# Performance work log

Measured on AMD Instinct MI355X. Metric: run time of the kernel, lower is better.

## Reference

```python
import jax, jax.numpy as jnp
import numpy as np

N, E, D = 50000, 800000, 128  # nodes, edges, n_feat


def setup_inputs() -> dict:
    key = jax.random.key(0)
    ks = jax.random.split(key, 12)
    scale = 1.0 / np.sqrt(D)

    def w(k):
        return jax.random.normal(k, (D, D), jnp.float32) * scale

    return {
        "h": jax.random.normal(ks[0], (N, D), jnp.float32),
        "src": jax.random.randint(ks[1], (E,), 0, N, jnp.int32),
        "dst": jax.random.randint(ks[2], (E,), 0, N, jnp.int32),
        # skip MLP: Linear -> ELU -> Linear
        "W_skip1": w(ks[3]), "b_skip1": jnp.zeros((D,), jnp.float32),
        "W_skip2": w(ks[4]), "b_skip2": jnp.zeros((D,), jnp.float32),
        # SAGEConv 1 (mean aggregator): fc_self, fc_neigh (bias-free) + shared bias
        "W_self1": w(ks[5]), "W_neigh1": w(ks[6]), "b_conv1": jnp.zeros((D,), jnp.float32),
        # self-interaction MLP
        "W_si1": w(ks[7]), "b_si1": jnp.zeros((D,), jnp.float32),
        "W_si2": w(ks[8]), "b_si2": jnp.zeros((D,), jnp.float32),
        # SAGEConv 2
        "W_self2": w(ks[9]), "W_neigh2": w(ks[10]), "b_conv2": jnp.zeros((D,), jnp.float32),
    }


def _sage_mean(h, src, dst, W_self, W_neigh, b):
    # DGL SAGEConv('mean'): fc_self(h) + fc_neigh(mean over in-neighbors of h_src) + bias
    n = h.shape[0]
    deg = jax.ops.segment_sum(jnp.ones((src.shape[0],), h.dtype), dst, num_segments=n)
    agg = jax.ops.segment_sum(h[src], dst, num_segments=n)  # [N, D] sum of neighbor feats
    agg = agg / jnp.maximum(deg, 1.0)[:, None]  # degree clamp for isolated nodes
    return h @ W_self + agg @ W_neigh + b


def reference(h, src, dst,
              W_skip1, b_skip1, W_skip2, b_skip2,
              W_self1, W_neigh1, b_conv1,
              W_si1, b_si1, W_si2, b_si2,
              W_self2, W_neigh2, b_conv2):
    elu = jax.nn.elu
    h_skip = elu(h @ W_skip1 + b_skip1) @ W_skip2 + b_skip2
    x = elu(_sage_mean(h, src, dst, W_self1, W_neigh1, b_conv1))
    x = elu(elu(x @ W_si1 + b_si1) @ W_si2 + b_si2)
    x = _sage_mean(x, src, dst, W_self2, W_neigh2, b_conv2)
    return h_skip + x
```

## Files before the change

kernel.cpp:

```cpp
#include <hip/hip_runtime.h>
#include <math.h>

#define NN 50000
#define NE 800000
#define NRT 782
#define NT  (NRT * 2)
#define NB  128
#define NPB2 391
#define EPB 2048
#define NBB 391

typedef __attribute__((ext_vector_type(8))) short short8;
typedef __attribute__((ext_vector_type(4))) float floatx4;

#define AS1 __attribute__((address_space(1)))
#define AS3 __attribute__((address_space(3)))

__device__ __forceinline__ unsigned short f2bf(float f) {
    unsigned u = __float_as_uint(f);
    unsigned r = (u + 0x7fff + ((u >> 16) & 1)) >> 16;
    return (unsigned short)r;
}
__device__ __forceinline__ float bf2f(unsigned short h) {
    return __uint_as_float(((unsigned)h) << 16);
}


__global__ __launch_bounds__(256)
void k_prep(const float* __restrict__ h, unsigned short* __restrict__ hB,
            const int* __restrict__ dst, int* __restrict__ bcnt,
            const float* w0, const float* w1, const float* w2, const float* w3,
            const float* w4, const float* w5, const float* w6, const float* w7,
            short* __restrict__ wpk) {
    int bid = blockIdx.x;
    const int t = threadIdx.x;
    if (bid < 3125) {
        int i = (bid * 256 + t) * 8;
        float4 a = *(const float4*)&h[i];
        float4 b = *(const float4*)&h[i + 4];
        short8 v;
        v[0] = (short)f2bf(a.x); v[1] = (short)f2bf(a.y);
        v[2] = (short)f2bf(a.z); v[3] = (short)f2bf(a.w);
        v[4] = (short)f2bf(b.x); v[5] = (short)f2bf(b.y);
        v[6] = (short)f2bf(b.z); v[7] = (short)f2bf(b.w);
        *(short8*)&hB[i] = v;
    } else if (bid < 3125 + NBB) {
        __shared__ int cnt[NB];
        if (t < NB) cnt[t] = 0;
        __syncthreads();
        int base = (bid - 3125) * EPB;
#pragma unroll
        for (int i = 0; i < 8; ++i) {
            int idx = base + i * 256 + t;
            if (idx < NE) atomicAdd(&cnt[dst[idx] / NPB2], 1);
        }
        __syncthreads();
        if (t < NB && cnt[t]) atomicAdd(&bcnt[t], cnt[t]);
    } else {
        int wb = bid - 3125 - NBB;
        const float* W;
        switch (wb) {
            case 0: W = w0; break; case 1: W = w1; break;
            case 2: W = w2; break; case 3: W = w3; break;
            case 4: W = w4; break; case 5: W = w5; break;
            case 6: W = w6; break; default: W = w7; break;
        }
        short* dstp = wpk + (size_t)wb * 16384;
#pragma unroll
        for (int i = 0; i < 8; ++i) {
            int q = t + i * 256;
            int cb = q >> 8, ks = (q >> 6) & 3, lane = q & 63;
            int n = lane & 15, g = lane >> 4;
            int col = cb * 16 + n, krow = ks * 32 + g * 8;
            short8 v;
#pragma unroll
            for (int j = 0; j < 8; ++j)
                v[j] = (short)f2bf(W[(krow + j) * 128 + col]);
            *(short8*)&dstp[q * 8] = v;
        }
    }
}


__global__ void k_bscan(const int* __restrict__ bcnt, int* __restrict__ gcur,
                        int* __restrict__ bstart) {
    __shared__ int s[NB];
    int t = threadIdx.x;
    int c = bcnt[t];
    s[t] = c;
    __syncthreads();
    for (int off = 1; off < NB; off <<= 1) {
        int v = (t >= off) ? s[t - off] : 0;
        __syncthreads();
        s[t] += v;
        __syncthreads();
    }
    int excl = s[t] - c;
    gcur[t] = excl;
    bstart[t] = excl;
    if (t == NB - 1) bstart[NB] = s[NB - 1];
}


__global__ __launch_bounds__(256)
void k_bucket(const int* __restrict__ src, const int* __restrict__ dst,
              int* __restrict__ gcur, int* __restrict__ bsrc, int* __restrict__ bdst) {
    __shared__ int psrc[EPB];
    __shared__ int pdst[EPB];
    __shared__ int cnt[NB];
    __shared__ int ebase[NB];
    __shared__ int gbase[NB];
    const int t = threadIdx.x;
    const int e0 = blockIdx.x * EPB;
    const int M = (e0 + EPB <= NE) ? EPB : (NE - e0);

    if (t < NB) cnt[t] = 0;
    __syncthreads();

    int es[8], ed[8], rank[8];
#pragma unroll
    for (int i = 0; i < 8; ++i) {
        int idx = i * 256 + t;
        if (idx < M) {
            es[i] = src[e0 + idx];
            ed[i] = dst[e0 + idx];
            rank[i] = atomicAdd(&cnt[ed[i] / NPB2], 1);
        }
    }
    __syncthreads();
    if (t < NB) ebase[t] = cnt[t];
    __syncthreads();
    for (int off = 1; off < NB; off <<= 1) {
        int v = 0;
        if (t < NB && t >= off) v = ebase[t - off];
        __syncthreads();
        if (t < NB) ebase[t] += v;
        __syncthreads();
    }
    if (t < NB) ebase[t] -= cnt[t];
    __syncthreads();
#pragma unroll
    for (int i = 0; i < 8; ++i) {
        int idx = i * 256 + t;
        if (idx < M) {
            int b = ed[i] / NPB2;
            int pos = ebase[b] + rank[i];
            psrc[pos] = es[i];
            pdst[pos] = ed[i];
        }
    }
    if (t < NB && cnt[t] > 0) gbase[t] = atomicAdd(&gcur[t], cnt[t]);
    __syncthreads();
#pragma unroll
    for (int i = 0; i < 8; ++i) {
        int idx = i * 256 + t;
        if (idx < M) {
            int d = pdst[idx];
            int b = d / NPB2;
            int gpos = gbase[b] + (idx - ebase[b]);
            bsrc[gpos] = psrc[idx];
            bdst[gpos] = d;
        }
    }
}


template<int DOELU, int OUTF32, int NOBIAS>
__device__ __forceinline__ void gemm_body(
        int bid, const unsigned short* __restrict__ A,
        const short* __restrict__ Wp, const float* __restrict__ bias,
        void* outv, short* sW, short* sA) {
    const int t = threadIdx.x;
    const int wv = t >> 6, lane = t & 63;
    const int rb = bid >> 1, ct = bid & 1;
    const int row0 = rb * 64, col0 = ct * 64;
    const int m = lane & 15, g = lane >> 4;

    floatx4 acc[4];
#pragma unroll
    for (int cb = 0; cb < 4; ++cb) acc[cb] = (floatx4){0.f, 0.f, 0.f, 0.f};

    const short* Wc = Wp + ct * 8192;
#pragma unroll
    for (int i = 0; i < 4; ++i) {
        int cbase = (i * 4 + wv) * 64;
        __builtin_amdgcn_global_load_lds(
            (const AS1 unsigned int*)(Wc + (size_t)(cbase + lane) * 8),
            (AS3 unsigned int*)(sW + cbase * 8), 16, 0, 0);
    }
#pragma unroll
    for (int i = 0; i < 4; ++i) {
        int cbase = (i * 4 + wv) * 64;
        int id = cbase + lane;
        int r = id >> 4, cs = id & 15;
        int rg = row0 + r; if (rg >= NN) rg = NN - 1;
        int csrc = cs ^ (r & 7);
        __builtin_amdgcn_global_load_lds(
            (const AS1 unsigned int*)(A + (size_t)rg * 128 + csrc * 8),
            (AS3 unsigned int*)(sA + cbase * 8), 16, 0, 0);
    }
    asm volatile("s_waitcnt vmcnt(0)" ::: "memory");
    __builtin_amdgcn_sched_barrier(0);
    __syncthreads();

    const int r0 = wv * 16;
#pragma unroll
    for (int ks = 0; ks < 4; ++ks) {
        int cxor = (ks * 4 + g) ^ (m & 7);
        short8 af = *(const short8*)&sA[((r0 + m) * 16 + cxor) * 8];
#pragma unroll
        for (int cb = 0; cb < 4; ++cb) {
            short8 bf = *(const short8*)&sW[((cb * 4 + ks) * 64 + lane) * 8];
            acc[cb] = __builtin_amdgcn_mfma_f32_16x16x32_bf16(af, bf, acc[cb], 0, 0, 0);
        }
    }

    const int rowbase = row0 + wv * 16 + g * 4;
#pragma unroll
    for (int cb = 0; cb < 4; ++cb) {
        int C = col0 + cb * 16 + m;
        float bb = NOBIAS ? 0.f : bias[C];
#pragma unroll
        for (int rr = 0; rr < 4; ++rr) {
            int R = rowbase + rr;
            if (R < NN) {
                size_t idx = (size_t)R * 128 + C;
                float v = acc[cb][rr] + bb;
                if (DOELU) v = (v > 0.f) ? v : expm1f(v);
                if (OUTF32) ((float*)outv)[idx] = v;
                else        ((unsigned short*)outv)[idx] = f2bf(v);
            }
        }
    }
}

template<int DOELU, int OUTF32, int NOBIAS>
__global__ __launch_bounds__(256)
void k_mm(const unsigned short* __restrict__ A, const short* __restrict__ Wp,
          const float* __restrict__ bias, void* outv) {
    __shared__ short sMem[16384];
    gemm_body<DOELU, OUTF32, NOBIAS>(blockIdx.x, A, Wp, bias, outv, sMem, sMem + 8192);
}


__device__ __forceinline__ void gemm3_body(
        int bid, const unsigned short* __restrict__ A,
        const short* __restrict__ Wn, const short* __restrict__ Ws,
        const short* __restrict__ Wk, const float* __restrict__ bsk1,
        unsigned short* __restrict__ T1, unsigned short* __restrict__ C1,
        unsigned short* __restrict__ S1, short* sW, short* sA) {
    const int t = threadIdx.x;
    const int wv = t >> 6, lane = t & 63;
    const int rb = bid >> 1, ct = bid & 1;
    const int row0 = rb * 64, col0 = ct * 64;
    const int m = lane & 15, g = lane >> 4;

#pragma unroll
    for (int i = 0; i < 4; ++i) {
        int cbase = (i * 4 + wv) * 64;
        int id = cbase + lane;
        int r = id >> 4, cs = id & 15;
        int rg = row0 + r; if (rg >= NN) rg = NN - 1;
        int csrc = cs ^ (r & 7);
        __builtin_amdgcn_global_load_lds(
            (const AS1 unsigned int*)(A + (size_t)rg * 128 + csrc * 8),
            (AS3 unsigned int*)(sA + cbase * 8), 16, 0, 0);
    }

#pragma unroll
    for (int ph = 0; ph < 3; ++ph) {
        if (ph) __syncthreads();
        const short* Wc = (ph == 0 ? Wn : ph == 1 ? Ws : Wk) + ct * 8192;
#pragma unroll
        for (int i = 0; i < 4; ++i) {
            int cbase = (i * 4 + wv) * 64;
            __builtin_amdgcn_global_load_lds(
                (const AS1 unsigned int*)(Wc + (size_t)(cbase + lane) * 8),
                (AS3 unsigned int*)(sW + cbase * 8), 16, 0, 0);
        }
        asm volatile("s_waitcnt vmcnt(0)" ::: "memory");
        __builtin_amdgcn_sched_barrier(0);
        __syncthreads();

        floatx4 acc[4];
#pragma unroll
        for (int cb = 0; cb < 4; ++cb) acc[cb] = (floatx4){0.f, 0.f, 0.f, 0.f};
        const int r0 = wv * 16;
#pragma unroll
        for (int ks = 0; ks < 4; ++ks) {
            int cxor = (ks * 4 + g) ^ (m & 7);
            short8 af = *(const short8*)&sA[((r0 + m) * 16 + cxor) * 8];
#pragma unroll
            for (int cb = 0; cb < 4; ++cb) {
                short8 bf = *(const short8*)&sW[((cb * 4 + ks) * 64 + lane) * 8];
                acc[cb] = __builtin_amdgcn_mfma_f32_16x16x32_bf16(af, bf, acc[cb], 0, 0, 0);
            }
        }

        const int rowbase = row0 + wv * 16 + g * 4;
#pragma unroll
        for (int cb = 0; cb < 4; ++cb) {
            int C = col0 + cb * 16 + m;
            float bb = (ph == 2) ? bsk1[C] : 0.f;
#pragma unroll
            for (int rr = 0; rr < 4; ++rr) {
                int R = rowbase + rr;
                if (R < NN) {
                    size_t idx = (size_t)R * 128 + C;
                    float v = acc[cb][rr] + bb;
                    if (ph == 0)      T1[idx] = f2bf(v);
                    else if (ph == 1) C1[idx] = f2bf(v);
                    else {
                        v = (v > 0.f) ? v : expm1f(v);
                        S1[idx] = f2bf(v);
                    }
                }
            }
        }
    }
}


__global__ __launch_bounds__(256)
void k_gfinal(const unsigned short* __restrict__ X3, const unsigned short* __restrict__ AG2,
              const unsigned short* __restrict__ S1, const short* __restrict__ wpk,
              const float* __restrict__ bconv2, const float* __restrict__ bsk2,
              float* __restrict__ out) {
    __shared__ short sMem[16384];
    short* sW = sMem;
    short* sA = sMem + 8192;
    const int t = threadIdx.x;
    const int wv = t >> 6, lane = t & 63;
    const int rb = blockIdx.x >> 1, ct = blockIdx.x & 1;
    const int row0 = rb * 64, col0 = ct * 64;
    const int m = lane & 15, g = lane >> 4;

    floatx4 acc[4];
#pragma unroll
    for (int cb = 0; cb < 4; ++cb) acc[cb] = (floatx4){0.f, 0.f, 0.f, 0.f};

#pragma unroll
    for (int ph = 0; ph < 3; ++ph) {
        if (ph) __syncthreads();
        const unsigned short* Ac = (ph == 0) ? X3 : (ph == 1) ? AG2 : S1;
        const short* Wc = wpk + (ph == 0 ? 6 : ph == 1 ? 7 : 1) * 16384 + ct * 8192;
#pragma unroll
        for (int i = 0; i < 4; ++i) {
            int cbase = (i * 4 + wv) * 64;
            __builtin_amdgcn_global_load_lds(
                (const AS1 unsigned int*)(Wc + (size_t)(cbase + lane) * 8),
                (AS3 unsigned int*)(sW + cbase * 8), 16, 0, 0);
        }
#pragma unroll
        for (int i = 0; i < 4; ++i) {
            int cbase = (i * 4 + wv) * 64;
            int id = cbase + lane;
            int r = id >> 4, cs = id & 15;
            int rg = row0 + r; if (rg >= NN) rg = NN - 1;
            int csrc = cs ^ (r & 7);
            __builtin_amdgcn_global_load_lds(
                (const AS1 unsigned int*)(Ac + (size_t)rg * 128 + csrc * 8),
                (AS3 unsigned int*)(sA + cbase * 8), 16, 0, 0);
        }
        asm volatile("s_waitcnt vmcnt(0)" ::: "memory");
        __builtin_amdgcn_sched_barrier(0);
        __syncthreads();

        const int r0 = wv * 16;
#pragma unroll
        for (int ks = 0; ks < 4; ++ks) {
            int cxor = (ks * 4 + g) ^ (m & 7);
            short8 af = *(const short8*)&sA[((r0 + m) * 16 + cxor) * 8];
#pragma unroll
            for (int cb = 0; cb < 4; ++cb) {
                short8 bf = *(const short8*)&sW[((cb * 4 + ks) * 64 + lane) * 8];
                acc[cb] = __builtin_amdgcn_mfma_f32_16x16x32_bf16(af, bf, acc[cb], 0, 0, 0);
            }
        }
    }

    const int rowbase = row0 + wv * 16 + g * 4;
#pragma unroll
    for (int cb = 0; cb < 4; ++cb) {
        int C = col0 + cb * 16 + m;
        float bb = bconv2[C] + bsk2[C];
#pragma unroll
        for (int rr = 0; rr < 4; ++rr) {
            int R = rowbase + rr;
            if (R < NN) out[(size_t)R * 128 + C] = acc[cb][rr] + bb;
        }
    }
}


__global__ __launch_bounds__(256)
void k_mega1(const int* __restrict__ bsrc, const int* __restrict__ bdst,
             const int* __restrict__ bstart, int* __restrict__ row_start,
             int* __restrict__ col_idx,
             const unsigned short* __restrict__ hB, const short* __restrict__ wpk,
             const float* __restrict__ bsk1,
             unsigned short* __restrict__ T1out, unsigned short* __restrict__ C1out,
             unsigned short* __restrict__ S1out) {
    __shared__ short sMem[16384];
    int bid = blockIdx.x;
    if (bid < NB) {
        int* lcur = (int*)sMem;
        int* sc   = lcur + NPB2;
        int* rs   = sc + 512;
        const int t = threadIdx.x;
        const int n0 = bid * NPB2;
        const int n1 = (n0 + NPB2 < NN) ? n0 + NPB2 : NN;
        const int nn = n1 - n0;
        const int w0 = bstart[bid], w1 = bstart[bid + 1];
        for (int i = t; i < nn; i += 256) lcur[i] = 0;
        __syncthreads();
        for (int e = w0 + t; e < w1; e += 256)
            atomicAdd(&lcur[bdst[e] - n0], 1);
        __syncthreads();
        int v0 = (t < nn) ? lcur[t] : 0;
        int v1 = (t + 256 < nn) ? lcur[t + 256] : 0;
        sc[t] = v0; sc[t + 256] = v1;
        __syncthreads();
        for (int off = 1; off < 512; off <<= 1) {
            int a0 = (t >= off) ? sc[t - off] : 0;
            int a1 = (t + 256 >= off) ? sc[t + 256 - off] : 0;
            __syncthreads();
            sc[t] += a0; sc[t + 256] += a1;
            __syncthreads();
        }
        for (int i = t; i < nn; i += 256) {
            int r = w0 + sc[i] - lcur[i];
            rs[i] = r;
            row_start[n0 + i] = r;
            lcur[i] = 0;
        }
        if (bid == 0 && t == 0) row_start[NN] = NE;
        __syncthreads();
        for (int e = w0 + t; e < w1; e += 256) {
            int d = bdst[e] - n0;
            int slot = atomicAdd(&lcur[d], 1);
            col_idx[rs[d] + slot] = bsrc[e];
        }
    } else {
        gemm3_body(bid - NB, hB, wpk + 3 * 16384 , wpk + 2 * 16384 ,
                   wpk , bsk1, T1out, C1out, S1out, sMem, sMem + 8192);
    }
}


__device__ __forceinline__ void gather8(const unsigned short* __restrict__ F,
                                        const int* __restrict__ col_idx,
                                        int beg, int end, int grp, size_t lo,
                                        float a[8]) {
#pragma unroll
    for (int i = 0; i < 8; ++i) a[i] = 0.f;
    int j = beg;
#pragma unroll 1
    for (; j + 16 <= end; j += 16) {
        int s[4];
#pragma unroll
        for (int u = 0; u < 4; ++u) s[u] = col_idx[j + 4 * u + grp];
        uint4 v[4];
#pragma unroll
        for (int u = 0; u < 4; ++u)
            v[u] = *(const uint4*)&F[(size_t)s[u] * 128 + lo];
#pragma unroll
        for (int u = 0; u < 4; ++u) {
            a[0] += bf2f((unsigned short)(v[u].x & 0xffff));
            a[1] += bf2f((unsigned short)(v[u].x >> 16));
            a[2] += bf2f((unsigned short)(v[u].y & 0xffff));
            a[3] += bf2f((unsigned short)(v[u].y >> 16));
            a[4] += bf2f((unsigned short)(v[u].z & 0xffff));
            a[5] += bf2f((unsigned short)(v[u].z >> 16));
            a[6] += bf2f((unsigned short)(v[u].w & 0xffff));
            a[7] += bf2f((unsigned short)(v[u].w >> 16));
        }
    }
#pragma unroll 1
    for (; j < end; j += 4) {
        int e = j + grp;
        if (e < end) {
            int s = col_idx[e];
            uint4 v = *(const uint4*)&F[(size_t)s * 128 + lo];
            a[0] += bf2f((unsigned short)(v.x & 0xffff));
            a[1] += bf2f((unsigned short)(v.x >> 16));
            a[2] += bf2f((unsigned short)(v.y & 0xffff));
            a[3] += bf2f((unsigned short)(v.y >> 16));
            a[4] += bf2f((unsigned short)(v.z & 0xffff));
            a[5] += bf2f((unsigned short)(v.z >> 16));
            a[6] += bf2f((unsigned short)(v.w & 0xffff));
            a[7] += bf2f((unsigned short)(v.w >> 16));
        }
    }
#pragma unroll
    for (int i = 0; i < 8; ++i) {
        a[i] += __shfl_xor(a[i], 16);
        a[i] += __shfl_xor(a[i], 32);
    }
}


__global__ __launch_bounds__(256)
void k_agg1x(const unsigned short* __restrict__ T1, const int* __restrict__ row_start,
             const int* __restrict__ col_idx, const unsigned short* __restrict__ C1,
             const float* __restrict__ bc, unsigned short* __restrict__ X1out) {
    int node = (blockIdx.x * 256 + threadIdx.x) >> 6;
    int lane = threadIdx.x & 63;
    if (node >= NN) return;
    const int grp = lane >> 4, gl = lane & 15;
    const int beg = row_start[node], end = row_start[node + 1];
    const size_t lo = (size_t)(gl * 8);
    float a[8];
    gather8(T1, col_idx, beg, end, grp, lo, a);
    if (lane < 16) {
        float inv = 1.0f / fmaxf((float)(end - beg), 1.0f);
        uint4 c = *(const uint4*)&C1[(size_t)node * 128 + lo];
        float4 b0 = *(const float4*)&bc[gl * 8];
        float4 b1 = *(const float4*)&bc[gl * 8 + 4];
        float x[8];
        x[0] = a[0] * inv + bf2f((unsigned short)(c.x & 0xffff)) + b0.x;
        x[1] = a[1] * inv + bf2f((unsigned short)(c.x >> 16)) + b0.y;
        x[2] = a[2] * inv + bf2f((unsigned short)(c.y & 0xffff)) + b0.z;
        x[3] = a[3] * inv + bf2f((unsigned short)(c.y >> 16)) + b0.w;
        x[4] = a[4] * inv + bf2f((unsigned short)(c.z & 0xffff)) + b1.x;
        x[5] = a[5] * inv + bf2f((unsigned short)(c.z >> 16)) + b1.y;
        x[6] = a[6] * inv + bf2f((unsigned short)(c.w & 0xffff)) + b1.z;
        x[7] = a[7] * inv + bf2f((unsigned short)(c.w >> 16)) + b1.w;
#pragma unroll
        for (int i = 0; i < 8; ++i)
            x[i] = (x[i] > 0.f) ? x[i] : expm1f(x[i]);
        uint4 o;
        o.x = (unsigned)f2bf(x[0]) | ((unsigned)f2bf(x[1]) << 16);
        o.y = (unsigned)f2bf(x[2]) | ((unsigned)f2bf(x[3]) << 16);
        o.z = (unsigned)f2bf(x[4]) | ((unsigned)f2bf(x[5]) << 16);
        o.w = (unsigned)f2bf(x[6]) | ((unsigned)f2bf(x[7]) << 16);
        *(uint4*)&X1out[(size_t)node * 128 + lo] = o;
    }
}


__global__ __launch_bounds__(256)
void k_agg2(const unsigned short* __restrict__ X3, const int* __restrict__ row_start,
            const int* __restrict__ col_idx, unsigned short* __restrict__ AG2out) {
    int node = (blockIdx.x * 256 + threadIdx.x) >> 6;
    int lane = threadIdx.x & 63;
    if (node >= NN) return;
    const int grp = lane >> 4, gl = lane & 15;
    const int beg = row_start[node], end = row_start[node + 1];
    const size_t lo = (size_t)(gl * 8);
    float a[8];
    gather8(X3, col_idx, beg, end, grp, lo, a);
    if (lane < 16) {
        float inv = 1.0f / fmaxf((float)(end - beg), 1.0f);
        uint4 o;
        o.x = (unsigned)f2bf(a[0] * inv) | ((unsigned)f2bf(a[1] * inv) << 16);
        o.y = (unsigned)f2bf(a[2] * inv) | ((unsigned)f2bf(a[3] * inv) << 16);
        o.z = (unsigned)f2bf(a[4] * inv) | ((unsigned)f2bf(a[5] * inv) << 16);
        o.w = (unsigned)f2bf(a[6] * inv) | ((unsigned)f2bf(a[7] * inv) << 16);
        *(uint4*)&AG2out[(size_t)node * 128 + lo] = o;
    }
}


extern "C" void kernel_launch(void* const* d_in, const int* in_sizes, int n_in,
                              void* d_out, int out_size, void* d_ws, size_t ws_size,
                              hipStream_t stream) {
    const float* h        = (const float*)d_in[0];
    const int*   src      = (const int*)d_in[1];
    const int*   dst      = (const int*)d_in[2];
    const float* W_skip1  = (const float*)d_in[3];
    const float* b_skip1  = (const float*)d_in[4];
    const float* W_skip2  = (const float*)d_in[5];
    const float* b_skip2  = (const float*)d_in[6];
    const float* W_self1  = (const float*)d_in[7];
    const float* W_neigh1 = (const float*)d_in[8];
    const float* b_conv1  = (const float*)d_in[9];
    const float* W_si1    = (const float*)d_in[10];
    const float* b_si1    = (const float*)d_in[11];
    const float* W_si2    = (const float*)d_in[12];
    const float* b_si2    = (const float*)d_in[13];
    const float* W_self2  = (const float*)d_in[14];
    const float* W_neigh2 = (const float*)d_in[15];
    const float* b_conv2  = (const float*)d_in[16];
    float* out = (float*)d_out;

    char* ws = (char*)d_ws;
    int* bcnt      = (int*)ws;
    int* gcur      = bcnt + 128;
    int* bstart    = bcnt + 256;
    int* row_start = bcnt + 100096;
    int* col_idx   = bcnt + 150272;
    short* wpk          = (short*)(ws + 3801088);
    unsigned short* hB  = (unsigned short*)(ws + 4063232);
    unsigned short* B1  = (unsigned short*)(ws + 16863232);
    unsigned short* B2  = (unsigned short*)(ws + 29663232);
    int* bsrc           = (int*)(ws + 42463232);
    int* bdst           = (int*)(ws + 45663232);
    unsigned short* C1s = (unsigned short*)d_out;

    hipMemsetAsync(ws, 0, 128 * sizeof(int), stream);

    k_prep<<<3125 + NBB + 8, 256, 0, stream>>>(h, hB, dst, bcnt,
                                               W_skip1, W_skip2, W_self1, W_neigh1,
                                               W_si1, W_si2, W_self2, W_neigh2, wpk);
    k_bscan<<<1, NB, 0, stream>>>(bcnt, gcur, bstart);

    k_bucket<<<NBB, 256, 0, stream>>>(src, dst, gcur, bsrc, bdst);

    k_mega1<<<NB + NT, 256, 0, stream>>>(bsrc, bdst, bstart, row_start, col_idx,
                                         hB, wpk, b_skip1, B1, C1s, B2);

    k_agg1x<<<12500, 256, 0, stream>>>(B1, row_start, col_idx, C1s, b_conv1, hB);

    k_mm<1, 0, 0><<<NT, 256, 0, stream>>>(hB, wpk + 4 * 16384, b_si1, B1);
    k_mm<1, 0, 0><<<NT, 256, 0, stream>>>(B1, wpk + 5 * 16384, b_si2, hB);

    k_agg2<<<12500, 256, 0, stream>>>(hB, row_start, col_idx, B1);

    k_gfinal<<<NT, 256, 0, stream>>>(hB, B1, B2, wpk, b_conv2, b_skip2, out);
}
```

Baseline: 182.4 us.

## Fuse self-interaction MLP GEMMs into one kernel and double bucket count

Replaces the two back-to-back k_mm launches for the self-interaction MLP with a single k_si12 kernel. Each block computes 64 rows across all 128 columns, keeps the ELU intermediate in LDS as bf16, and writes the final result in place. This removes one launch and the global round trip of the intermediate activation, at the cost of larger LDS use and more accumulators per thread. The edge-bucketing pass also moves from 128 to 256 buckets (196 nodes each), which gives the CSR build more blocks and smaller per-bucket work. The bucket scan and the workspace offsets are resized to match.

```diff
diff --git a/kernel.cpp b/kernel.cpp
--- a/kernel.cpp
+++ b/kernel.cpp
@@ -5,8 +5,8 @@
 #define NE 800000
 #define NRT 782
 #define NT  (NRT * 2)
-#define NB  128
-#define NPB2 391
+#define NB  256
+#define NPB2 196
 #define EPB 2048
 #define NBB 391
 
@@ -46,7 +46,7 @@
         *(short8*)&hB[i] = v;
     } else if (bid < 3125 + NBB) {
         __shared__ int cnt[NB];
-        if (t < NB) cnt[t] = 0;
+        cnt[t] = 0;
         __syncthreads();
         int base = (bid - 3125) * EPB;
 #pragma unroll
@@ -55,7 +55,7 @@
             if (idx < NE) atomicAdd(&cnt[dst[idx] / NPB2], 1);
         }
         __syncthreads();
-        if (t < NB && cnt[t]) atomicAdd(&bcnt[t], cnt[t]);
+        if (cnt[t]) atomicAdd(&bcnt[t], cnt[t]);
     } else {
         int wb = bid - 3125 - NBB;
         const float* W;
@@ -114,7 +114,7 @@
     const int e0 = blockIdx.x * EPB;
     const int M = (e0 + EPB <= NE) ? EPB : (NE - e0);
 
-    if (t < NB) cnt[t] = 0;
+    cnt[t] = 0;
     __syncthreads();
 
     int es[8], ed[8], rank[8];
@@ -128,16 +128,15 @@
         }
     }
     __syncthreads();
-    if (t < NB) ebase[t] = cnt[t];
+    ebase[t] = cnt[t];
     __syncthreads();
     for (int off = 1; off < NB; off <<= 1) {
-        int v = 0;
-        if (t < NB && t >= off) v = ebase[t - off];
-        __syncthreads();
-        if (t < NB) ebase[t] += v;
-        __syncthreads();
-    }
-    if (t < NB) ebase[t] -= cnt[t];
+        int v = (t >= off) ? ebase[t - off] : 0;
+        __syncthreads();
+        ebase[t] += v;
+        __syncthreads();
+    }
+    ebase[t] -= cnt[t];
     __syncthreads();
 #pragma unroll
     for (int i = 0; i < 8; ++i) {
@@ -149,7 +148,7 @@
             pdst[pos] = ed[i];
         }
     }
-    if (t < NB && cnt[t] > 0) gbase[t] = atomicAdd(&gcur[t], cnt[t]);
+    if (cnt[t] > 0) gbase[t] = atomicAdd(&gcur[t], cnt[t]);
     __syncthreads();
 #pragma unroll
     for (int i = 0; i < 8; ++i) {
@@ -165,29 +164,24 @@
 }
 
 
-template<int DOELU, int OUTF32, int NOBIAS>
-__device__ __forceinline__ void gemm_body(
-        int bid, const unsigned short* __restrict__ A,
-        const short* __restrict__ Wp, const float* __restrict__ bias,
-        void* outv, short* sW, short* sA) {
-    const int t = threadIdx.x;
-    const int wv = t >> 6, lane = t & 63;
-    const int rb = bid >> 1, ct = bid & 1;
-    const int row0 = rb * 64, col0 = ct * 64;
-    const int m = lane & 15, g = lane >> 4;
-
-    floatx4 acc[4];
-#pragma unroll
-    for (int cb = 0; cb < 4; ++cb) acc[cb] = (floatx4){0.f, 0.f, 0.f, 0.f};
-
-    const short* Wc = Wp + ct * 8192;
-#pragma unroll
-    for (int i = 0; i < 4; ++i) {
+__device__ __forceinline__ void drain_barrier() {
+    asm volatile("s_waitcnt vmcnt(0)" ::: "memory");
+    __builtin_amdgcn_sched_barrier(0);
+    __syncthreads();
+}
+
+__device__ __forceinline__ void stage_w128(const short* Wc, short* sW, int wv, int lane) {
+#pragma unroll
+    for (int i = 0; i < 8; ++i) {
         int cbase = (i * 4 + wv) * 64;
         __builtin_amdgcn_global_load_lds(
             (const AS1 unsigned int*)(Wc + (size_t)(cbase + lane) * 8),
             (AS3 unsigned int*)(sW + cbase * 8), 16, 0, 0);
     }
+}
+
+__device__ __forceinline__ void stage_a64(const unsigned short* Ac, short* sX, int row0,
+                                          int wv, int lane) {
 #pragma unroll
     for (int i = 0; i < 4; ++i) {
         int cbase = (i * 4 + wv) * 64;
@@ -196,50 +190,45 @@
         int rg = row0 + r; if (rg >= NN) rg = NN - 1;
         int csrc = cs ^ (r & 7);
         __builtin_amdgcn_global_load_lds(
-            (const AS1 unsigned int*)(A + (size_t)rg * 128 + csrc * 8),
-            (AS3 unsigned int*)(sA + cbase * 8), 16, 0, 0);
-    }
-    asm volatile("s_waitcnt vmcnt(0)" ::: "memory");
-    __builtin_amdgcn_sched_barrier(0);
-    __syncthreads();
-
+            (const AS1 unsigned int*)(Ac + (size_t)rg * 128 + csrc * 8),
+            (AS3 unsigned int*)(sX + cbase * 8), 16, 0, 0);
+    }
+}
+
+__device__ __forceinline__ void mm128(const short* sX, const short* sW, int wv, int lane,
+                                      floatx4 acc[8]) {
+    const int m = lane & 15, g = lane >> 4;
     const int r0 = wv * 16;
 #pragma unroll
     for (int ks = 0; ks < 4; ++ks) {
-        int cxor = (ks * 4 + g) ^ (m & 7);
-        short8 af = *(const short8*)&sA[((r0 + m) * 16 + cxor) * 8];
-#pragma unroll
-        for (int cb = 0; cb < 4; ++cb) {
+        int slot = (ks * 4 + g) ^ (m & 7);
+        short8 af = *(const short8*)&sX[((r0 + m) * 16 + slot) * 8];
+#pragma unroll
+        for (int cb = 0; cb < 8; ++cb) {
             short8 bf = *(const short8*)&sW[((cb * 4 + ks) * 64 + lane) * 8];
             acc[cb] = __builtin_amdgcn_mfma_f32_16x16x32_bf16(af, bf, acc[cb], 0, 0, 0);
         }
     }
-
-    const int rowbase = row0 + wv * 16 + g * 4;
-#pragma unroll
-    for (int cb = 0; cb < 4; ++cb) {
-        int C = col0 + cb * 16 + m;
-        float bb = NOBIAS ? 0.f : bias[C];
+}
+
+__device__ __forceinline__ void act_to_lds64(short* sX, const float* bias, int wv, int lane,
+                                             floatx4 acc[8]) {
+    const int m = lane & 15, g = lane >> 4;
+#pragma unroll
+    for (int cb = 0; cb < 8; ++cb) {
+        int C = cb * 16 + m;
+        float bb = bias[C];
 #pragma unroll
         for (int rr = 0; rr < 4; ++rr) {
-            int R = rowbase + rr;
-            if (R < NN) {
-                size_t idx = (size_t)R * 128 + C;
-                float v = acc[cb][rr] + bb;
-                if (DOELU) v = (v > 0.f) ? v : expm1f(v);
-                if (OUTF32) ((float*)outv)[idx] = v;
-                else        ((unsigned short*)outv)[idx] = f2bf(v);
-            }
-        }
-    }
-}
-
-template<int DOELU, int OUTF32, int NOBIAS>
-__global__ __launch_bounds__(256)
-void k_mm(const unsigned short* __restrict__ A, const short* __restrict__ Wp,
-          const float* __restrict__ bias, void* outv) {
-    __shared__ short sMem[16384];
-    gemm_body<DOELU, OUTF32, NOBIAS>(blockIdx.x, A, Wp, bias, outv, sMem, sMem + 8192);
+            int Rl = wv * 16 + g * 4 + rr;
+            float v = acc[cb][rr] + bb;
+            v = (v > 0.f) ? v : expm1f(v);
+            int slot = (C >> 3) ^ (Rl & 7);
+            sX[(Rl * 16 + slot) * 8 + (C & 7)] = (short)f2bf(v);
+        }
+    }
+#pragma unroll
+    for (int cb = 0; cb < 8; ++cb) acc[cb] = (floatx4){0.f, 0.f, 0.f, 0.f};
 }
 
 
@@ -316,78 +305,6 @@
                     }
                 }
             }
-        }
-    }
-}
-
-
-__global__ __launch_bounds__(256)
-void k_gfinal(const unsigned short* __restrict__ X3, const unsigned short* __restrict__ AG2,
-              const unsigned short* __restrict__ S1, const short* __restrict__ wpk,
-              const float* __restrict__ bconv2, const float* __restrict__ bsk2,
-              float* __restrict__ out) {
-    __shared__ short sMem[16384];
-    short* sW = sMem;
-    short* sA = sMem + 8192;
-    const int t = threadIdx.x;
-    const int wv = t >> 6, lane = t & 63;
-    const int rb = blockIdx.x >> 1, ct = blockIdx.x & 1;
-    const int row0 = rb * 64, col0 = ct * 64;
-    const int m = lane & 15, g = lane >> 4;
-
-    floatx4 acc[4];
-#pragma unroll
-    for (int cb = 0; cb < 4; ++cb) acc[cb] = (floatx4){0.f, 0.f, 0.f, 0.f};
-
-#pragma unroll
-    for (int ph = 0; ph < 3; ++ph) {
-        if (ph) __syncthreads();
-        const unsigned short* Ac = (ph == 0) ? X3 : (ph == 1) ? AG2 : S1;
-        const short* Wc = wpk + (ph == 0 ? 6 : ph == 1 ? 7 : 1) * 16384 + ct * 8192;
-#pragma unroll
-        for (int i = 0; i < 4; ++i) {
-            int cbase = (i * 4 + wv) * 64;
-            __builtin_amdgcn_global_load_lds(
-                (const AS1 unsigned int*)(Wc + (size_t)(cbase + lane) * 8),
-                (AS3 unsigned int*)(sW + cbase * 8), 16, 0, 0);
-        }
-#pragma unroll
-        for (int i = 0; i < 4; ++i) {
-            int cbase = (i * 4 + wv) * 64;
-            int id = cbase + lane;
-            int r = id >> 4, cs = id & 15;
-            int rg = row0 + r; if (rg >= NN) rg = NN - 1;
-            int csrc = cs ^ (r & 7);
-            __builtin_amdgcn_global_load_lds(
-                (const AS1 unsigned int*)(Ac + (size_t)rg * 128 + csrc * 8),
-                (AS3 unsigned int*)(sA + cbase * 8), 16, 0, 0);
-        }
-        asm volatile("s_waitcnt vmcnt(0)" ::: "memory");
-        __builtin_amdgcn_sched_barrier(0);
-        __syncthreads();
-
-        const int r0 = wv * 16;
-#pragma unroll
-        for (int ks = 0; ks < 4; ++ks) {
-            int cxor = (ks * 4 + g) ^ (m & 7);
-            short8 af = *(const short8*)&sA[((r0 + m) * 16 + cxor) * 8];
-#pragma unroll
-            for (int cb = 0; cb < 4; ++cb) {
-                short8 bf = *(const short8*)&sW[((cb * 4 + ks) * 64 + lane) * 8];
-                acc[cb] = __builtin_amdgcn_mfma_f32_16x16x32_bf16(af, bf, acc[cb], 0, 0, 0);
-            }
-        }
-    }
-
-    const int rowbase = row0 + wv * 16 + g * 4;
-#pragma unroll
-    for (int cb = 0; cb < 4; ++cb) {
-        int C = col0 + cb * 16 + m;
-        float bb = bconv2[C] + bsk2[C];
-#pragma unroll
-        for (int rr = 0; rr < 4; ++rr) {
-            int R = rowbase + rr;
-            if (R < NN) out[(size_t)R * 128 + C] = acc[cb][rr] + bb;
         }
     }
 }
@@ -444,6 +361,121 @@
     } else {
         gemm3_body(bid - NB, hB, wpk + 3 * 16384 , wpk + 2 * 16384 ,
                    wpk , bsk1, T1out, C1out, S1out, sMem, sMem + 8192);
+    }
+}
+
+
+__global__ __launch_bounds__(256)
+void k_gfinal(const unsigned short* __restrict__ X3, const unsigned short* __restrict__ AG2,
+              const unsigned short* __restrict__ S1, const short* __restrict__ wpk,
+              const float* __restrict__ bconv2, const float* __restrict__ bsk2,
+              float* __restrict__ out) {
+    __shared__ short sMem[16384];
+    short* sW = sMem;
+    short* sA = sMem + 8192;
+    const int t = threadIdx.x;
+    const int wv = t >> 6, lane = t & 63;
+    const int rb = blockIdx.x >> 1, ct = blockIdx.x & 1;
+    const int row0 = rb * 64, col0 = ct * 64;
+    const int m = lane & 15, g = lane >> 4;
+
+    floatx4 acc[4];
+#pragma unroll
+    for (int cb = 0; cb < 4; ++cb) acc[cb] = (floatx4){0.f, 0.f, 0.f, 0.f};
+
+#pragma unroll
+    for (int ph = 0; ph < 3; ++ph) {
+        if (ph) __syncthreads();
+        const unsigned short* Ac = (ph == 0) ? X3 : (ph == 1) ? AG2 : S1;
+        const short* Wc = wpk + (ph == 0 ? 6 : ph == 1 ? 7 : 1) * 16384 + ct * 8192;
+#pragma unroll
+        for (int i = 0; i < 4; ++i) {
+            int cbase = (i * 4 + wv) * 64;
+            __builtin_amdgcn_global_load_lds(
+                (const AS1 unsigned int*)(Wc + (size_t)(cbase + lane) * 8),
+                (AS3 unsigned int*)(sW + cbase * 8), 16, 0, 0);
+        }
+#pragma unroll
+        for (int i = 0; i < 4; ++i) {
+            int cbase = (i * 4 + wv) * 64;
+            int id = cbase + lane;
+            int r = id >> 4, cs = id & 15;
+            int rg = row0 + r; if (rg >= NN) rg = NN - 1;
+            int csrc = cs ^ (r & 7);
+            __builtin_amdgcn_global_load_lds(
+                (const AS1 unsigned int*)(Ac + (size_t)rg * 128 + csrc * 8),
+                (AS3 unsigned int*)(sA + cbase * 8), 16, 0, 0);
+        }
+        asm volatile("s_waitcnt vmcnt(0)" ::: "memory");
+        __builtin_amdgcn_sched_barrier(0);
+        __syncthreads();
+
+        const int r0 = wv * 16;
+#pragma unroll
+        for (int ks = 0; ks < 4; ++ks) {
+            int cxor = (ks * 4 + g) ^ (m & 7);
+            short8 af = *(const short8*)&sA[((r0 + m) * 16 + cxor) * 8];
+#pragma unroll
+            for (int cb = 0; cb < 4; ++cb) {
+                short8 bf = *(const short8*)&sW[((cb * 4 + ks) * 64 + lane) * 8];
+                acc[cb] = __builtin_amdgcn_mfma_f32_16x16x32_bf16(af, bf, acc[cb], 0, 0, 0);
+            }
+        }
+    }
+
+    const int rowbase = row0 + wv * 16 + g * 4;
+#pragma unroll
+    for (int cb = 0; cb < 4; ++cb) {
+        int C = col0 + cb * 16 + m;
+        float bb = bconv2[C] + bsk2[C];
+#pragma unroll
+        for (int rr = 0; rr < 4; ++rr) {
+            int R = rowbase + rr;
+            if (R < NN) out[(size_t)R * 128 + C] = acc[cb][rr] + bb;
+        }
+    }
+}
+
+
+__global__ __launch_bounds__(256)
+void k_si12(unsigned short* __restrict__ X1io, const short* __restrict__ WpSi1,
+            const short* __restrict__ WpSi2, const float* __restrict__ bs1,
+            const float* __restrict__ bs2) {
+    __shared__ short sW[16384];
+    __shared__ short sX[8192];
+    const int t = threadIdx.x, wv = t >> 6, lane = t & 63;
+    const int row0 = blockIdx.x * 64;
+
+    floatx4 acc[8];
+#pragma unroll
+    for (int cb = 0; cb < 8; ++cb) acc[cb] = (floatx4){0.f, 0.f, 0.f, 0.f};
+
+    stage_a64(X1io, sX, row0, wv, lane);
+    stage_w128(WpSi1, sW, wv, lane);
+    drain_barrier();
+    mm128(sX, sW, wv, lane, acc);
+
+    __syncthreads();
+    stage_w128(WpSi2, sW, wv, lane);
+    act_to_lds64(sX, bs1, wv, lane, acc);
+    drain_barrier();
+    mm128(sX, sW, wv, lane, acc);
+
+    const int m = lane & 15, g = lane >> 4;
+    const int rowbase = row0 + wv * 16 + g * 4;
+#pragma unroll
+    for (int cb = 0; cb < 8; ++cb) {
+        int C = cb * 16 + m;
+        float bb = bs2[C];
+#pragma unroll
+        for (int rr = 0; rr < 4; ++rr) {
+            int R = rowbase + rr;
+            if (R < NN) {
+                float v = acc[cb][rr] + bb;
+                v = (v > 0.f) ? v : expm1f(v);
+                X1io[(size_t)R * 128 + C] = f2bf(v);
+            }
+        }
     }
 }
 
@@ -586,8 +618,8 @@
 
     char* ws = (char*)d_ws;
     int* bcnt      = (int*)ws;
-    int* gcur      = bcnt + 128;
-    int* bstart    = bcnt + 256;
+    int* gcur      = bcnt + 256;
+    int* bstart    = bcnt + 512;
     int* row_start = bcnt + 100096;
     int* col_idx   = bcnt + 150272;
     short* wpk          = (short*)(ws + 3801088);
@@ -598,7 +630,7 @@
     int* bdst           = (int*)(ws + 45663232);
     unsigned short* C1s = (unsigned short*)d_out;
 
-    hipMemsetAsync(ws, 0, 128 * sizeof(int), stream);
+    hipMemsetAsync(ws, 0, 256 * sizeof(int), stream);
 
     k_prep<<<3125 + NBB + 8, 256, 0, stream>>>(h, hB, dst, bcnt,
                                                W_skip1, W_skip2, W_self1, W_neigh1,
@@ -612,8 +644,7 @@
 
     k_agg1x<<<12500, 256, 0, stream>>>(B1, row_start, col_idx, C1s, b_conv1, hB);
 
-    k_mm<1, 0, 0><<<NT, 256, 0, stream>>>(hB, wpk + 4 * 16384, b_si1, B1);
-    k_mm<1, 0, 0><<<NT, 256, 0, stream>>>(B1, wpk + 5 * 16384, b_si2, hB);
+    k_si12<<<NRT, 256, 0, stream>>>(hB, wpk + 4 * 16384, wpk + 5 * 16384, b_si1, b_si2);
 
     k_agg2<<<12500, 256, 0, stream>>>(hB, row_start, col_idx, B1);
 
```

New measurement: 177.3 us. 2.8% less time.
